# Kernel tuning notes

Measured on AMD Instinct MI355X. Metric: run time of the kernel, lower is better.

## Reference

```python
import jax, jax.numpy as jnp
import numpy as np

BS, S, DIM, H = 4, 2048, 768, 12
DH = DIM // H  # 64


def setup_inputs() -> dict:
    key = jax.random.key(0)
    ks = jax.random.split(key, 12)
    std = 0.02
    inp = {
        "query": jax.random.normal(ks[0], (BS, S, DIM), jnp.float32),
        "key_t": jax.random.normal(ks[1], (BS, S, DIM), jnp.float32),
        "value": jax.random.normal(ks[2], (BS, S, DIM), jnp.float32),
        "mask": jnp.ones((BS, S), jnp.int32),
        "q_w": jax.random.normal(ks[3], (DIM, DIM), jnp.float32) * std,
        "q_b": jnp.zeros((DIM,), jnp.float32),
        "k_w": jax.random.normal(ks[4], (DIM, DIM), jnp.float32) * std,
        "k_b": jnp.zeros((DIM,), jnp.float32),
        "v_w": jax.random.normal(ks[5], (DIM, DIM), jnp.float32) * std,
        "v_b": jnp.zeros((DIM,), jnp.float32),
        "o_w": jax.random.normal(ks[6], (DIM, DIM), jnp.float32) * std,
        "o_b": jnp.zeros((DIM,), jnp.float32),
    }
    return inp


def _shape(x, bs):
    # (bs, L, dim) -> (bs, H, L, DH)
    return x.reshape(bs, -1, H, DH).transpose(0, 2, 1, 3)


def reference(query, key_t, value, mask, q_w, q_b, k_w, k_b, v_w, v_b, o_w, o_b):
    bs, q_len, _ = query.shape
    k_len = key_t.shape[1]
    q = _shape(query @ q_w.T + q_b, bs)   # (bs,H,Sq,DH)
    k = _shape(key_t @ k_w.T + k_b, bs)   # (bs,H,Sk,DH)
    v = _shape(value @ v_w.T + v_b, bs)
    q = q * (1.0 / jnp.sqrt(jnp.asarray(DH, q.dtype)))
    scores = jnp.einsum("bhqd,bhkd->bhqk", q, k)  # (bs,H,Sq,Sk)
    pad = (mask == 0)[:, None, None, :]           # (bs,1,1,Sk)
    neg = jnp.finfo(scores.dtype).min
    scores = jnp.where(pad, neg, scores)
    weights = jax.nn.softmax(scores, axis=-1)
    context = jnp.einsum("bhqk,bhkd->bhqd", weights, v)
    context = context.transpose(0, 2, 1, 3).reshape(bs, q_len, H * DH)
    out = context @ o_w.T + o_b
    return out
```

## Files before the change

kernel.cpp:

```cpp
#include <hip/hip_runtime.h>


#define BSZ 4
#define SEQ 2048
#define DIMD 768
#define NHD 12
#define MTOT (BSZ*SEQ)
#define WELEM (DIMD*DIMD)

typedef __bf16 bf16;
typedef __attribute__((ext_vector_type(8))) __bf16 bf16x8;
typedef __attribute__((ext_vector_type(4))) __bf16 bf16x4;
typedef __attribute__((ext_vector_type(4))) float f32x4;

__device__ __forceinline__ f32x4 mfma_bf16(bf16x8 a, bf16x8 b, f32x4 c) {
    return __builtin_amdgcn_mfma_f32_16x16x32_bf16(a, b, c, 0, 0, 0);
}

__device__ __forceinline__ void async16(const bf16* g, bf16* l) {
    __builtin_amdgcn_global_load_lds(
        (const __attribute__((address_space(1))) unsigned int*)g,
        (__attribute__((address_space(3))) unsigned int*)l, 16, 0, 0);
}

__global__ __launch_bounds__(256) void convert_w_kernel(
    const float* __restrict__ w0, const float* __restrict__ w1,
    const float* __restrict__ w2, const float* __restrict__ w3,
    bf16* __restrict__ out) {
    const int z = blockIdx.y;
    const float* src = (z == 0) ? w0 : (z == 1) ? w1 : (z == 2) ? w2 : w3;
    const int i = (blockIdx.x * 256 + threadIdx.x) * 4;
    float4 v = *(const float4*)(src + i);
    bf16x4 o;
    o[0] = (bf16)v.x; o[1] = (bf16)v.y; o[2] = (bf16)v.z; o[3] = (bf16)v.w;
    *(bf16x4*)(out + (size_t)z * WELEM + i) = o;
}

__global__ __launch_bounds__(256) void convert_x_kernel(
    const float* __restrict__ src, bf16* __restrict__ dst) {
    const int i = (blockIdx.x * 256 + threadIdx.x) * 4;
    float4 v = *(const float4*)(src + i);
    bf16x4 o;
    o[0] = (bf16)v.x; o[1] = (bf16)v.y; o[2] = (bf16)v.z; o[3] = (bf16)v.w;
    *(bf16x4*)(dst + i) = o;
}

__device__ __forceinline__ void gemm_core_768(
    const bf16* __restrict__ Ag, const bf16* __restrict__ Bg,
    int m0, int n0, bf16* As, bf16* Bs, f32x4 (&acc)[4][4]) {
    const int tid = threadIdx.x;
    const int lane = tid & 63, wv = tid >> 6;
    const int quad = lane >> 4, l16 = lane & 15;
    const int wr = wv >> 1, wc = wv & 1;
    const int rr = lane >> 3, cbl = lane & 7;
    const int swz = l16 & 7;
    for (int kt = 0; kt < 12; ++kt) {
        if (kt) __syncthreads();
        for (int c = 0; c < 4; ++c) {
            const int row = c * 32 + wv * 8 + rr;
            const int cb = cbl ^ (row & 7);
            const size_t gcol = (size_t)kt * 64 + cb * 8;
            async16(Ag + (size_t)(m0 + row) * 768 + gcol, As + row * 64 + cbl * 8);
            async16(Bg + (size_t)(n0 + row) * 768 + gcol, Bs + row * 64 + cbl * 8);
        }
        __syncthreads();
        for (int ks = 0; ks < 2; ++ks) {
            bf16x8 af[4], bfr[4];
            for (int t = 0; t < 4; ++t)
                af[t] = *(const bf16x8*)(As + (wr * 64 + t * 16 + l16) * 64 +
                                         (((ks * 4 + quad) ^ swz) * 8));
            for (int t = 0; t < 4; ++t)
                bfr[t] = *(const bf16x8*)(Bs + (wc * 64 + t * 16 + l16) * 64 +
                                          (((ks * 4 + quad) ^ swz) * 8));
            for (int ti = 0; ti < 4; ++ti)
                for (int tj = 0; tj < 4; ++tj)
                    acc[ti][tj] = mfma_bf16(af[ti], bfr[tj], acc[ti][tj]);
        }
    }
}

__global__ __launch_bounds__(256, 3) void proj_kernel(
    const bf16* __restrict__ X, const bf16* __restrict__ W,
    const float* __restrict__ bias, bf16* __restrict__ Out, int z) {
    __shared__ __align__(16) bf16 smem[2 * 128 * 64];
    bf16* As = smem;
    bf16* Bs = smem + 128 * 64;
    const int tid = threadIdx.x;
    const int lane = tid & 63, wv = tid >> 6;
    const int quad = lane >> 4, l16 = lane & 15;
    const int wr = wv >> 1, wc = wv & 1;
    f32x4 acc[4][4] = {};
    int m0, n0;
    const bf16 *Ag, *Bg;
    if (z < 2) { m0 = blockIdx.y * 128; n0 = blockIdx.x * 128; Ag = W; Bg = X; }
    else       { m0 = blockIdx.x * 128; n0 = blockIdx.y * 128; Ag = X; Bg = W; }
    gemm_core_768(Ag, Bg, m0, n0, As, Bs, acc);
    __syncthreads();
    bf16* Ot = smem;
    if (z < 2) {
        const float scale = (z == 0) ? 0.125f : 1.0f;
        for (int ti = 0; ti < 4; ++ti) {
            const int featl = wr * 64 + ti * 16 + quad * 4;
            const float4 b4 = *(const float4*)(bias + m0 + featl);
            for (int tj = 0; tj < 4; ++tj) {
                const int sl = wc * 64 + tj * 16 + l16;
                bf16x4 pk;
                pk[0] = (bf16)((acc[ti][tj][0] + b4.x) * scale);
                pk[1] = (bf16)((acc[ti][tj][1] + b4.y) * scale);
                pk[2] = (bf16)((acc[ti][tj][2] + b4.z) * scale);
                pk[3] = (bf16)((acc[ti][tj][3] + b4.w) * scale);
                *(bf16x4*)&Ot[sl * 128 + featl] = pk;
            }
        }
        __syncthreads();
        for (int it = 0; it < 8; ++it) {
            const int unit = it * 256 + tid;
            const int s = unit >> 4, u = unit & 15;
            const int feat = m0 + u * 8;
            const int hh = feat >> 6, dh = feat & 63;
            const int srow = n0 + s;
            const int bb = srow >> 11, s2 = srow & 2047;
            *(bf16x8*)&Out[((size_t)(bb * NHD + hh) * SEQ + s2) * 64 + dh] =
                *(const bf16x8*)&Ot[s * 128 + u * 8];
        }
    } else {
        for (int ti = 0; ti < 4; ++ti) {
            const int sl = wr * 64 + ti * 16 + quad * 4;
            for (int tj = 0; tj < 4; ++tj) {
                const int featl = wc * 64 + tj * 16 + l16;
                const float bv = bias[n0 + featl];
                bf16x4 pk;
                pk[0] = (bf16)(acc[ti][tj][0] + bv);
                pk[1] = (bf16)(acc[ti][tj][1] + bv);
                pk[2] = (bf16)(acc[ti][tj][2] + bv);
                pk[3] = (bf16)(acc[ti][tj][3] + bv);
                *(bf16x4*)&Ot[featl * 128 + sl] = pk;
            }
        }
        __syncthreads();
        const int bb = m0 >> 11, sbase = m0 & 2047;
        for (int it = 0; it < 8; ++it) {
            const int unit = it * 256 + tid;
            const int fl = unit >> 4, u = unit & 15;
            const int feat = n0 + fl;
            const int hh = feat >> 6, dh = feat & 63;
            *(bf16x8*)&Out[((size_t)(bb * NHD + hh) * 64 + dh) * SEQ + sbase + u * 8] =
                *(const bf16x8*)&Ot[fl * 128 + u * 8];
        }
    }
}

__global__ __launch_bounds__(256, 3) void attn_kernel(
    const bf16* __restrict__ Qb, const bf16* __restrict__ Kb, const bf16* __restrict__ Vb,
    const int* __restrict__ mask, bf16* __restrict__ CTX) {
    __shared__ __align__(16) bf16 Ps[2][128][72];
    __shared__ float alphas[2][128];
    __shared__ float sadd[2048];
    __shared__ float invs[128];
    __shared__ int anyz_s;
    const int tid = threadIdx.x;
    const int lane = tid & 63, wv = tid >> 6, quad = lane >> 4, l16 = lane & 15;
    const int b = blockIdx.z, h = blockIdx.y, qt = blockIdx.x;
    const int bh = b * NHD + h;
    if (tid == 0) anyz_s = 0;
    __syncthreads();
    {
        int4 m0v = *(const int4*)(mask + b * SEQ + tid * 8);
        int4 m1v = *(const int4*)(mask + b * SEQ + tid * 8 + 4);
        float4 f0, f1;
        f0.x = m0v.x ? 0.f : -1e30f; f0.y = m0v.y ? 0.f : -1e30f;
        f0.z = m0v.z ? 0.f : -1e30f; f0.w = m0v.w ? 0.f : -1e30f;
        f1.x = m1v.x ? 0.f : -1e30f; f1.y = m1v.y ? 0.f : -1e30f;
        f1.z = m1v.z ? 0.f : -1e30f; f1.w = m1v.w ? 0.f : -1e30f;
        *(float4*)&sadd[tid * 8] = f0;
        *(float4*)&sadd[tid * 8 + 4] = f1;
        if (!(m0v.x && m0v.y && m0v.z && m0v.w && m1v.x && m1v.y && m1v.z && m1v.w))
            anyz_s = 1;
    }
    bf16x8 qf0[2], qf1[2];
    for (int st = 0; st < 2; ++st) {
        const bf16* qp = Qb + ((size_t)bh * SEQ + qt * 128 + wv * 32 + st * 16 + l16) * 64;
        qf0[st] = *(const bf16x8*)(qp + quad * 8);
        qf1[st] = *(const bf16x8*)(qp + 32 + quad * 8);
    }
    const bf16* Kp = Kb + (size_t)bh * SEQ * 64 + (size_t)l16 * 64 + quad * 8;
    const bf16* Vp = Vb + (size_t)bh * 64 * SEQ + (size_t)(wv * 16 + l16) * SEQ + quad * 8;
    f32x4 acc_o[8] = {};
    float rm[2] = {-1e30f, -1e30f}, rs[2] = {0.f, 0.f};
    __syncthreads();
    const int az = anyz_s;
    for (int kt = 0; kt < SEQ / 64; ++kt) {
        const int buf = kt & 1, k0 = kt * 64;
        bf16x8 kf0[4], kf1[4];
        for (int jj = 0; jj < 4; ++jj) {
            const bf16* kp = Kp + (size_t)(k0 + jj * 16) * 64;
            kf0[jj] = *(const bf16x8*)kp;
            kf1[jj] = *(const bf16x8*)(kp + 32);
        }
        f32x4 sc[2][4];
        for (int st = 0; st < 2; ++st)
            for (int jj = 0; jj < 4; ++jj) {
                f32x4 zf = {};
                zf = mfma_bf16(kf0[jj], qf0[st], zf);
                sc[st][jj] = mfma_bf16(kf1[jj], qf1[st], zf);
            }
        if (az)
            for (int jj = 0; jj < 4; ++jj) {
                const float4 sa = *(const float4*)&sadd[k0 + jj * 16 + quad * 4];
                for (int st = 0; st < 2; ++st) {
                    sc[st][jj][0] += sa.x; sc[st][jj][1] += sa.y;
                    sc[st][jj][2] += sa.z; sc[st][jj][3] += sa.w;
                }
            }
        for (int st = 0; st < 2; ++st) {
            float tmax = -1e30f;
            for (int jj = 0; jj < 4; ++jj)
                for (int r = 0; r < 4; ++r) tmax = fmaxf(tmax, sc[st][jj][r]);
            tmax = fmaxf(tmax, __shfl_xor(tmax, 16));
            tmax = fmaxf(tmax, __shfl_xor(tmax, 32));
            const float nmax = fmaxf(rm[st], tmax);
            const float alpha = __expf(rm[st] - nmax);
            rm[st] = nmax;
            float tsum = 0.f;
            for (int jj = 0; jj < 4; ++jj) {
                bf16x4 pk;
                for (int r = 0; r < 4; ++r) {
                    const float p = __expf(sc[st][jj][r] - nmax);
                    tsum += p;
                    pk[r] = (bf16)p;
                }
                *(bf16x4*)&Ps[buf][wv * 32 + st * 16 + l16][jj * 16 + quad * 4] = pk;
            }
            tsum += __shfl_xor(tsum, 16);
            tsum += __shfl_xor(tsum, 32);
            rs[st] = rs[st] * alpha + tsum;
            if (lane < 16) alphas[buf][wv * 32 + st * 16 + lane] = alpha;
        }
        bf16x8 vf0 = *(const bf16x8*)(Vp + k0);
        bf16x8 vf1 = *(const bf16x8*)(Vp + k0 + 32);
        __syncthreads();
        for (int qj = 0; qj < 8; ++qj) {
            const float al = alphas[buf][qj * 16 + l16];
            f32x4 c = acc_o[qj];
            c[0] *= al; c[1] *= al; c[2] *= al; c[3] *= al;
            bf16x8 pf0 = *(const bf16x8*)&Ps[buf][qj * 16 + l16][quad * 8];
            bf16x8 pf1 = *(const bf16x8*)&Ps[buf][qj * 16 + l16][32 + quad * 8];
            c = mfma_bf16(vf0, pf0, c);
            c = mfma_bf16(vf1, pf1, c);
            acc_o[qj] = c;
        }
    }
    if (lane < 16) {
        invs[wv * 32 + lane] = 1.0f / rs[0];
        invs[wv * 32 + 16 + lane] = 1.0f / rs[1];
    }
    __syncthreads();
    for (int qj = 0; qj < 8; ++qj) {
        const float inv = invs[qj * 16 + l16];
        bf16x4 pk;
        for (int r = 0; r < 4; ++r) pk[r] = (bf16)(acc_o[qj][r] * inv);
        const int s = qt * 128 + qj * 16 + l16;
        *(bf16x4*)&CTX[(size_t)(b * SEQ + s) * DIMD + h * 64 + wv * 16 + quad * 4] = pk;
    }
}

__global__ __launch_bounds__(256, 3) void oproj_kernel(
    const bf16* __restrict__ ctx, const bf16* __restrict__ wo,
    const float* __restrict__ bo, float* __restrict__ out) {
    __shared__ __align__(16) bf16 smem[2 * 128 * 64];
    const int tid = threadIdx.x;
    const int lane = tid & 63, wv = tid >> 6;
    const int quad = lane >> 4, l16 = lane & 15;
    const int wr = wv >> 1, wc = wv & 1;
    const int m0 = blockIdx.x * 128, n0 = blockIdx.y * 128;
    f32x4 acc[4][4] = {};
    gemm_core_768(ctx, wo, m0, n0, smem, smem + 128 * 64, acc);
    for (int ti = 0; ti < 4; ++ti) {
        const int rowb = m0 + wr * 64 + ti * 16 + quad * 4;
        for (int tj = 0; tj < 4; ++tj) {
            const int feat = n0 + wc * 64 + tj * 16 + l16;
            const float bv = bo[feat];
            for (int r = 0; r < 4; ++r)
                out[(size_t)(rowb + r) * DIMD + feat] = acc[ti][tj][r] + bv;
        }
    }
}

extern "C" void kernel_launch(void* const* d_in, const int* in_sizes, int n_in,
                              void* d_out, int out_size, void* d_ws, size_t ws_size,
                              hipStream_t stream) {
    const float* query = (const float*)d_in[0];
    const float* key_t = (const float*)d_in[1];
    const float* value = (const float*)d_in[2];
    const int*   mask  = (const int*)d_in[3];
    const float* q_w = (const float*)d_in[4];
    const float* q_b = (const float*)d_in[5];
    const float* k_w = (const float*)d_in[6];
    const float* k_b = (const float*)d_in[7];
    const float* v_w = (const float*)d_in[8];
    const float* v_b = (const float*)d_in[9];
    const float* o_w = (const float*)d_in[10];
    const float* o_b = (const float*)d_in[11];
    float* out = (float*)d_out;

    bf16* ws  = (bf16*)d_ws;
    bf16* W   = ws;
    bf16* XB  = ws + (size_t)4 * WELEM;
    bf16* Qb  = XB + (size_t)MTOT * DIMD;
    bf16* Kb  = Qb + (size_t)MTOT * DIMD;
    bf16* Vb  = Kb + (size_t)MTOT * DIMD;
    bf16* CTX = XB;

    convert_w_kernel<<<dim3(WELEM / 1024, 4), 256, 0, stream>>>(q_w, k_w, v_w, o_w, W);

    convert_x_kernel<<<MTOT * DIMD / 1024, 256, 0, stream>>>(query, XB);
    proj_kernel<<<dim3(64, 6), 256, 0, stream>>>(XB, W, q_b, Qb, 0);
    convert_x_kernel<<<MTOT * DIMD / 1024, 256, 0, stream>>>(key_t, XB);
    proj_kernel<<<dim3(64, 6), 256, 0, stream>>>(XB, W + (size_t)WELEM, k_b, Kb, 1);
    convert_x_kernel<<<MTOT * DIMD / 1024, 256, 0, stream>>>(value, XB);
    proj_kernel<<<dim3(64, 6), 256, 0, stream>>>(XB, W + (size_t)2 * WELEM, v_b, Vb, 2);

    attn_kernel<<<dim3(SEQ / 128, NHD, BSZ), 256, 0, stream>>>(Qb, Kb, Vb, mask, CTX);
    oproj_kernel<<<dim3(64, 6), 256, 0, stream>>>(CTX, W + (size_t)3 * WELEM, o_b, out);
}
```

Measured before the change: 333.1 us.

## Batch QKV projections, prefetch K/V in attention, swizzle GEMM block order

```diff
diff --git a/kernel.cpp b/kernel.cpp
--- a/kernel.cpp
+++ b/kernel.cpp
@@ -37,7 +37,12 @@
 }
 
 __global__ __launch_bounds__(256) void convert_x_kernel(
-    const float* __restrict__ src, bf16* __restrict__ dst) {
+    const float* __restrict__ x0, const float* __restrict__ x1,
+    const float* __restrict__ x2,
+    bf16* __restrict__ d0, bf16* __restrict__ d1, bf16* __restrict__ d2) {
+    const int z = blockIdx.y;
+    const float* src = (z == 0) ? x0 : (z == 1) ? x1 : x2;
+    bf16* dst = (z == 0) ? d0 : (z == 1) ? d1 : d2;
     const int i = (blockIdx.x * 256 + threadIdx.x) * 4;
     float4 v = *(const float4*)(src + i);
     bf16x4 o;
@@ -80,11 +85,24 @@
 }
 
 __global__ __launch_bounds__(256, 3) void proj_kernel(
-    const bf16* __restrict__ X, const bf16* __restrict__ W,
-    const float* __restrict__ bias, bf16* __restrict__ Out, int z) {
+    const bf16* __restrict__ Xq, const bf16* __restrict__ Xk, const bf16* __restrict__ Xv,
+    const bf16* __restrict__ W,
+    const float* __restrict__ bq, const float* __restrict__ bk, const float* __restrict__ bv,
+    bf16* __restrict__ Qo, bf16* __restrict__ Ko, bf16* __restrict__ Vo) {
     __shared__ __align__(16) bf16 smem[2 * 128 * 64];
     bf16* As = smem;
     bf16* Bs = smem + 128 * 64;
+    const int lin = blockIdx.x;
+    const int swzb = (lin & 7) * 144 + (lin >> 3);
+    const int z = swzb / 384;
+    const int rem = swzb - z * 384;
+    const int rt = rem / 6;
+    const int xt = rem - rt * 6;
+    const bf16* X = (z == 0) ? Xq : (z == 1) ? Xk : Xv;
+    const bf16* Wz = W + (size_t)z * WELEM;
+    const float* bias = (z == 0) ? bq : (z == 1) ? bk : bv;
+    bf16* Out = (z == 0) ? Qo : (z == 1) ? Ko : Vo;
+
     const int tid = threadIdx.x;
     const int lane = tid & 63, wv = tid >> 6;
     const int quad = lane >> 4, l16 = lane & 15;
@@ -92,8 +110,8 @@
     f32x4 acc[4][4] = {};
     int m0, n0;
     const bf16 *Ag, *Bg;
-    if (z < 2) { m0 = blockIdx.y * 128; n0 = blockIdx.x * 128; Ag = W; Bg = X; }
-    else       { m0 = blockIdx.x * 128; n0 = blockIdx.y * 128; Ag = X; Bg = W; }
+    if (z < 2) { m0 = xt * 128; n0 = rt * 128; Ag = Wz; Bg = X; }
+    else       { m0 = rt * 128; n0 = xt * 128; Ag = X;  Bg = Wz; }
     gemm_core_768(Ag, Bg, m0, n0, As, Bs, acc);
     __syncthreads();
     bf16* Ot = smem;
@@ -155,7 +173,6 @@
     const int* __restrict__ mask, bf16* __restrict__ CTX) {
     __shared__ __align__(16) bf16 Ps[2][128][72];
     __shared__ float alphas[2][128];
-    __shared__ float sadd[2048];
     __shared__ float invs[128];
     __shared__ int anyz_s;
     const int tid = threadIdx.x;
@@ -167,13 +184,6 @@
     {
         int4 m0v = *(const int4*)(mask + b * SEQ + tid * 8);
         int4 m1v = *(const int4*)(mask + b * SEQ + tid * 8 + 4);
-        float4 f0, f1;
-        f0.x = m0v.x ? 0.f : -1e30f; f0.y = m0v.y ? 0.f : -1e30f;
-        f0.z = m0v.z ? 0.f : -1e30f; f0.w = m0v.w ? 0.f : -1e30f;
-        f1.x = m1v.x ? 0.f : -1e30f; f1.y = m1v.y ? 0.f : -1e30f;
-        f1.z = m1v.z ? 0.f : -1e30f; f1.w = m1v.w ? 0.f : -1e30f;
-        *(float4*)&sadd[tid * 8] = f0;
-        *(float4*)&sadd[tid * 8 + 4] = f1;
         if (!(m0v.x && m0v.y && m0v.z && m0v.w && m1v.x && m1v.y && m1v.z && m1v.w))
             anyz_s = 1;
     }
@@ -185,71 +195,97 @@
     }
     const bf16* Kp = Kb + (size_t)bh * SEQ * 64 + (size_t)l16 * 64 + quad * 8;
     const bf16* Vp = Vb + (size_t)bh * 64 * SEQ + (size_t)(wv * 16 + l16) * SEQ + quad * 8;
+    const int* Mp = mask + b * SEQ;
     f32x4 acc_o[8] = {};
     float rm[2] = {-1e30f, -1e30f}, rs[2] = {0.f, 0.f};
     __syncthreads();
     const int az = anyz_s;
-    for (int kt = 0; kt < SEQ / 64; ++kt) {
-        const int buf = kt & 1, k0 = kt * 64;
-        bf16x8 kf0[4], kf1[4];
-        for (int jj = 0; jj < 4; ++jj) {
-            const bf16* kp = Kp + (size_t)(k0 + jj * 16) * 64;
-            kf0[jj] = *(const bf16x8*)kp;
-            kf1[jj] = *(const bf16x8*)(kp + 32);
-        }
-        f32x4 sc[2][4];
-        for (int st = 0; st < 2; ++st)
-            for (int jj = 0; jj < 4; ++jj) {
-                f32x4 zf = {};
-                zf = mfma_bf16(kf0[jj], qf0[st], zf);
-                sc[st][jj] = mfma_bf16(kf1[jj], qf1[st], zf);
-            }
-        if (az)
-            for (int jj = 0; jj < 4; ++jj) {
-                const float4 sa = *(const float4*)&sadd[k0 + jj * 16 + quad * 4];
-                for (int st = 0; st < 2; ++st) {
-                    sc[st][jj][0] += sa.x; sc[st][jj][1] += sa.y;
-                    sc[st][jj][2] += sa.z; sc[st][jj][3] += sa.w;
-                }
-            }
-        for (int st = 0; st < 2; ++st) {
-            float tmax = -1e30f;
-            for (int jj = 0; jj < 4; ++jj)
-                for (int r = 0; r < 4; ++r) tmax = fmaxf(tmax, sc[st][jj][r]);
-            tmax = fmaxf(tmax, __shfl_xor(tmax, 16));
-            tmax = fmaxf(tmax, __shfl_xor(tmax, 32));
-            const float nmax = fmaxf(rm[st], tmax);
-            const float alpha = __expf(rm[st] - nmax);
-            rm[st] = nmax;
-            float tsum = 0.f;
-            for (int jj = 0; jj < 4; ++jj) {
-                bf16x4 pk;
-                for (int r = 0; r < 4; ++r) {
-                    const float p = __expf(sc[st][jj][r] - nmax);
-                    tsum += p;
-                    pk[r] = (bf16)p;
-                }
-                *(bf16x4*)&Ps[buf][wv * 32 + st * 16 + l16][jj * 16 + quad * 4] = pk;
-            }
-            tsum += __shfl_xor(tsum, 16);
-            tsum += __shfl_xor(tsum, 32);
-            rs[st] = rs[st] * alpha + tsum;
-            if (lane < 16) alphas[buf][wv * 32 + st * 16 + lane] = alpha;
-        }
-        bf16x8 vf0 = *(const bf16x8*)(Vp + k0);
-        bf16x8 vf1 = *(const bf16x8*)(Vp + k0 + 32);
-        __syncthreads();
-        for (int qj = 0; qj < 8; ++qj) {
-            const float al = alphas[buf][qj * 16 + l16];
-            f32x4 c = acc_o[qj];
-            c[0] *= al; c[1] *= al; c[2] *= al; c[3] *= al;
-            bf16x8 pf0 = *(const bf16x8*)&Ps[buf][qj * 16 + l16][quad * 8];
-            bf16x8 pf1 = *(const bf16x8*)&Ps[buf][qj * 16 + l16][32 + quad * 8];
-            c = mfma_bf16(vf0, pf0, c);
-            c = mfma_bf16(vf1, pf1, c);
-            acc_o[qj] = c;
-        }
-    }
+
+    bf16x8 kfa0[4], kfa1[4], vfa0, vfa1;
+    bf16x8 kfb0[4], kfb1[4], vfb0, vfb1;
+    for (int jj = 0; jj < 4; ++jj) {
+        const bf16* kp = Kp + (size_t)(jj * 16) * 64;
+        kfa0[jj] = *(const bf16x8*)kp;
+        kfa1[jj] = *(const bf16x8*)(kp + 32);
+    }
+    vfa0 = *(const bf16x8*)Vp;
+    vfa1 = *(const bf16x8*)(Vp + 32);
+
+#define ATT_STEP(KT, KC0, KC1, VC0, VC1, KN0, KN1, VN0, VN1) do {                  \
+        const int kt_ = (KT);                                                      \
+        const int buf_ = kt_ & 1;                                                  \
+        const int k0_ = kt_ * 64;                                                  \
+        f32x4 sc[2][4];                                                            \
+        for (int st = 0; st < 2; ++st)                                             \
+            for (int jj = 0; jj < 4; ++jj) {                                       \
+                f32x4 zf = {};                                                     \
+                zf = mfma_bf16(KC0[jj], qf0[st], zf);                              \
+                sc[st][jj] = mfma_bf16(KC1[jj], qf1[st], zf);                      \
+            }                                                                      \
+        {     \
+            const int kn_ = (kt_ + 1 < SEQ / 64) ? (kt_ + 1) * 64 : kt_ * 64;      \
+            for (int jj = 0; jj < 4; ++jj) {                                       \
+                const bf16* kp_ = Kp + (size_t)(kn_ + jj * 16) * 64;               \
+                KN0[jj] = *(const bf16x8*)kp_;                                     \
+                KN1[jj] = *(const bf16x8*)(kp_ + 32);                              \
+            }                                                                      \
+            VN0 = *(const bf16x8*)(Vp + kn_);                                      \
+            VN1 = *(const bf16x8*)(Vp + kn_ + 32);                                 \
+        }                                                                          \
+        if (az)                                                                    \
+            for (int jj = 0; jj < 4; ++jj) {                                       \
+                const int4 mm = *(const int4*)(Mp + k0_ + jj * 16 + quad * 4);     \
+                float4 sa;                                                         \
+                sa.x = mm.x ? 0.f : -1e30f; sa.y = mm.y ? 0.f : -1e30f;            \
+                sa.z = mm.z ? 0.f : -1e30f; sa.w = mm.w ? 0.f : -1e30f;            \
+                for (int st = 0; st < 2; ++st) {                                   \
+                    sc[st][jj][0] += sa.x; sc[st][jj][1] += sa.y;                  \
+                    sc[st][jj][2] += sa.z; sc[st][jj][3] += sa.w;                  \
+                }                                                                  \
+            }                                                                      \
+        for (int st = 0; st < 2; ++st) {                                           \
+            float tmax = -1e30f;                                                   \
+            for (int jj = 0; jj < 4; ++jj)                                         \
+                for (int r = 0; r < 4; ++r) tmax = fmaxf(tmax, sc[st][jj][r]);     \
+            tmax = fmaxf(tmax, __shfl_xor(tmax, 16));                              \
+            tmax = fmaxf(tmax, __shfl_xor(tmax, 32));                              \
+            const float nmax = fmaxf(rm[st], tmax);                                \
+            const float alpha = __expf(rm[st] - nmax);                             \
+            rm[st] = nmax;                                                         \
+            float tsum = 0.f;                                                      \
+            for (int jj = 0; jj < 4; ++jj) {                                       \
+                bf16x4 pk;                                                         \
+                for (int r = 0; r < 4; ++r) {                                      \
+                    const float p = __expf(sc[st][jj][r] - nmax);                  \
+                    tsum += p;                                                     \
+                    pk[r] = (bf16)p;                                               \
+                }                                                                  \
+                *(bf16x4*)&Ps[buf_][wv * 32 + st * 16 + l16][jj * 16 + quad * 4] = pk; \
+            }                                                                      \
+            tsum += __shfl_xor(tsum, 16);                                          \
+            tsum += __shfl_xor(tsum, 32);                                          \
+            rs[st] = rs[st] * alpha + tsum;                                        \
+            if (lane < 16) alphas[buf_][wv * 32 + st * 16 + lane] = alpha;         \
+        }                                                                          \
+        __syncthreads();                              \
+        for (int qj = 0; qj < 8; ++qj) {                                           \
+            const float al = alphas[buf_][qj * 16 + l16];                          \
+            f32x4 c = acc_o[qj];                                                   \
+            c[0] *= al; c[1] *= al; c[2] *= al; c[3] *= al;                        \
+            bf16x8 pf0 = *(const bf16x8*)&Ps[buf_][qj * 16 + l16][quad * 8];       \
+            bf16x8 pf1 = *(const bf16x8*)&Ps[buf_][qj * 16 + l16][32 + quad * 8];  \
+            c = mfma_bf16(VC0, pf0, c);                                            \
+            c = mfma_bf16(VC1, pf1, c);                                            \
+            acc_o[qj] = c;                                                         \
+        }                                                                          \
+    } while (0)
+
+    for (int kt2 = 0; kt2 < SEQ / 128; ++kt2) {
+        ATT_STEP(kt2 * 2,     kfa0, kfa1, vfa0, vfa1, kfb0, kfb1, vfb0, vfb1);
+        ATT_STEP(kt2 * 2 + 1, kfb0, kfb1, vfb0, vfb1, kfa0, kfa1, vfa0, vfa1);
+    }
+#undef ATT_STEP
+
     if (lane < 16) {
         invs[wv * 32 + lane] = 1.0f / rs[0];
         invs[wv * 32 + 16 + lane] = 1.0f / rs[1];
@@ -268,11 +304,15 @@
     const bf16* __restrict__ ctx, const bf16* __restrict__ wo,
     const float* __restrict__ bo, float* __restrict__ out) {
     __shared__ __align__(16) bf16 smem[2 * 128 * 64];
+    const int lin = blockIdx.x;
+    const int swzb = (lin & 7) * 48 + (lin >> 3);
+    const int rt = swzb / 6;
+    const int xt = swzb - rt * 6;
     const int tid = threadIdx.x;
     const int lane = tid & 63, wv = tid >> 6;
     const int quad = lane >> 4, l16 = lane & 15;
     const int wr = wv >> 1, wc = wv & 1;
-    const int m0 = blockIdx.x * 128, n0 = blockIdx.y * 128;
+    const int m0 = rt * 128, n0 = xt * 128;
     f32x4 acc[4][4] = {};
     gemm_core_768(ctx, wo, m0, n0, smem, smem + 128 * 64, acc);
     for (int ti = 0; ti < 4; ++ti) {
@@ -305,21 +345,20 @@
 
     bf16* ws  = (bf16*)d_ws;
     bf16* W   = ws;
-    bf16* XB  = ws + (size_t)4 * WELEM;
-    bf16* Qb  = XB + (size_t)MTOT * DIMD;
+    bf16* XBq = ws + (size_t)4 * WELEM;
+    bf16* XBk = XBq + (size_t)MTOT * DIMD;
+    bf16* XBv = XBk + (size_t)MTOT * DIMD;
+    bf16* Qb  = XBv + (size_t)MTOT * DIMD;
     bf16* Kb  = Qb + (size_t)MTOT * DIMD;
     bf16* Vb  = Kb + (size_t)MTOT * DIMD;
-    bf16* CTX = XB;
+    bf16* CTX = XBq;
 
     convert_w_kernel<<<dim3(WELEM / 1024, 4), 256, 0, stream>>>(q_w, k_w, v_w, o_w, W);
-
-    convert_x_kernel<<<MTOT * DIMD / 1024, 256, 0, stream>>>(query, XB);
-    proj_kernel<<<dim3(64, 6), 256, 0, stream>>>(XB, W, q_b, Qb, 0);
-    convert_x_kernel<<<MTOT * DIMD / 1024, 256, 0, stream>>>(key_t, XB);
-    proj_kernel<<<dim3(64, 6), 256, 0, stream>>>(XB, W + (size_t)WELEM, k_b, Kb, 1);
-    convert_x_kernel<<<MTOT * DIMD / 1024, 256, 0, stream>>>(value, XB);
-    proj_kernel<<<dim3(64, 6), 256, 0, stream>>>(XB, W + (size_t)2 * WELEM, v_b, Vb, 2);
+    convert_x_kernel<<<dim3(MTOT * DIMD / 1024, 3), 256, 0, stream>>>(
+        query, key_t, value, XBq, XBk, XBv);
+
+    proj_kernel<<<1152, 256, 0, stream>>>(XBq, XBk, XBv, W, q_b, k_b, v_b, Qb, Kb, Vb);
 
     attn_kernel<<<dim3(SEQ / 128, NHD, BSZ), 256, 0, stream>>>(Qb, Kb, Vb, mask, CTX);
-    oproj_kernel<<<dim3(64, 6), 256, 0, stream>>>(CTX, W + (size_t)3 * WELEM, o_b, out);
-}
+    oproj_kernel<<<384, 256, 0, stream>>>(CTX, W + (size_t)3 * WELEM, o_b, out);
+}
```

Result: faster. 312.5 us (-6.2%).

## Batch QKV projections, XCD-swizzle block order, per-wave attention without block syncs

Applied to the files above, without the earlier changes.

```diff
diff --git a/kernel.cpp b/kernel.cpp
--- a/kernel.cpp
+++ b/kernel.cpp
@@ -37,7 +37,12 @@
 }
 
 __global__ __launch_bounds__(256) void convert_x_kernel(
-    const float* __restrict__ src, bf16* __restrict__ dst) {
+    const float* __restrict__ x0, const float* __restrict__ x1,
+    const float* __restrict__ x2,
+    bf16* __restrict__ d0, bf16* __restrict__ d1, bf16* __restrict__ d2) {
+    const int z = blockIdx.y;
+    const float* src = (z == 0) ? x0 : (z == 1) ? x1 : x2;
+    bf16* dst = (z == 0) ? d0 : (z == 1) ? d1 : d2;
     const int i = (blockIdx.x * 256 + threadIdx.x) * 4;
     float4 v = *(const float4*)(src + i);
     bf16x4 o;
@@ -80,11 +85,24 @@
 }
 
 __global__ __launch_bounds__(256, 3) void proj_kernel(
-    const bf16* __restrict__ X, const bf16* __restrict__ W,
-    const float* __restrict__ bias, bf16* __restrict__ Out, int z) {
+    const bf16* __restrict__ Xq, const bf16* __restrict__ Xk, const bf16* __restrict__ Xv,
+    const bf16* __restrict__ W,
+    const float* __restrict__ bq, const float* __restrict__ bk, const float* __restrict__ bv,
+    bf16* __restrict__ Qo, bf16* __restrict__ Ko, bf16* __restrict__ Vo) {
     __shared__ __align__(16) bf16 smem[2 * 128 * 64];
     bf16* As = smem;
     bf16* Bs = smem + 128 * 64;
+    const int lin = blockIdx.x;
+    const int swzb = (lin & 7) * 144 + (lin >> 3);
+    const int z = swzb / 384;
+    const int rem = swzb - z * 384;
+    const int rt = rem / 6;
+    const int xt = rem - rt * 6;
+    const bf16* X = (z == 0) ? Xq : (z == 1) ? Xk : Xv;
+    const bf16* Wz = W + (size_t)z * WELEM;
+    const float* bias = (z == 0) ? bq : (z == 1) ? bk : bv;
+    bf16* Out = (z == 0) ? Qo : (z == 1) ? Ko : Vo;
+
     const int tid = threadIdx.x;
     const int lane = tid & 63, wv = tid >> 6;
     const int quad = lane >> 4, l16 = lane & 15;
@@ -92,8 +110,8 @@
     f32x4 acc[4][4] = {};
     int m0, n0;
     const bf16 *Ag, *Bg;
-    if (z < 2) { m0 = blockIdx.y * 128; n0 = blockIdx.x * 128; Ag = W; Bg = X; }
-    else       { m0 = blockIdx.x * 128; n0 = blockIdx.y * 128; Ag = X; Bg = W; }
+    if (z < 2) { m0 = xt * 128; n0 = rt * 128; Ag = Wz; Bg = X; }
+    else       { m0 = rt * 128; n0 = xt * 128; Ag = X;  Bg = Wz; }
     gemm_core_768(Ag, Bg, m0, n0, As, Bs, acc);
     __syncthreads();
     bf16* Ot = smem;
@@ -153,27 +171,20 @@
 __global__ __launch_bounds__(256, 3) void attn_kernel(
     const bf16* __restrict__ Qb, const bf16* __restrict__ Kb, const bf16* __restrict__ Vb,
     const int* __restrict__ mask, bf16* __restrict__ CTX) {
-    __shared__ __align__(16) bf16 Ps[2][128][72];
-    __shared__ float alphas[2][128];
-    __shared__ float sadd[2048];
-    __shared__ float invs[128];
+    __shared__ __align__(16) bf16 Ps[4][32][72];
     __shared__ int anyz_s;
     const int tid = threadIdx.x;
     const int lane = tid & 63, wv = tid >> 6, quad = lane >> 4, l16 = lane & 15;
-    const int b = blockIdx.z, h = blockIdx.y, qt = blockIdx.x;
-    const int bh = b * NHD + h;
+    const int lin = blockIdx.x;
+    const int nb = (lin & 7) * 96 + (lin >> 3);
+    const int qt = nb & 15;
+    const int bh = nb >> 4;
+    const int b = bh / NHD, h = bh - b * NHD;
     if (tid == 0) anyz_s = 0;
     __syncthreads();
     {
         int4 m0v = *(const int4*)(mask + b * SEQ + tid * 8);
         int4 m1v = *(const int4*)(mask + b * SEQ + tid * 8 + 4);
-        float4 f0, f1;
-        f0.x = m0v.x ? 0.f : -1e30f; f0.y = m0v.y ? 0.f : -1e30f;
-        f0.z = m0v.z ? 0.f : -1e30f; f0.w = m0v.w ? 0.f : -1e30f;
-        f1.x = m1v.x ? 0.f : -1e30f; f1.y = m1v.y ? 0.f : -1e30f;
-        f1.z = m1v.z ? 0.f : -1e30f; f1.w = m1v.w ? 0.f : -1e30f;
-        *(float4*)&sadd[tid * 8] = f0;
-        *(float4*)&sadd[tid * 8 + 4] = f1;
         if (!(m0v.x && m0v.y && m0v.z && m0v.w && m1v.x && m1v.y && m1v.z && m1v.w))
             anyz_s = 1;
     }
@@ -184,83 +195,105 @@
         qf1[st] = *(const bf16x8*)(qp + 32 + quad * 8);
     }
     const bf16* Kp = Kb + (size_t)bh * SEQ * 64 + (size_t)l16 * 64 + quad * 8;
-    const bf16* Vp = Vb + (size_t)bh * 64 * SEQ + (size_t)(wv * 16 + l16) * SEQ + quad * 8;
-    f32x4 acc_o[8] = {};
+    const bf16* Vp = Vb + (size_t)bh * 64 * SEQ + (size_t)l16 * SEQ + quad * 8;
+    const int* Mp = mask + b * SEQ;
+    bf16* Pw = &Ps[wv][0][0];
+    f32x4 acc[2][4] = {};
     float rm[2] = {-1e30f, -1e30f}, rs[2] = {0.f, 0.f};
     __syncthreads();
     const int az = anyz_s;
+
     for (int kt = 0; kt < SEQ / 64; ++kt) {
-        const int buf = kt & 1, k0 = kt * 64;
+        const int k0 = kt * 64;
         bf16x8 kf0[4], kf1[4];
+        #pragma unroll
         for (int jj = 0; jj < 4; ++jj) {
             const bf16* kp = Kp + (size_t)(k0 + jj * 16) * 64;
             kf0[jj] = *(const bf16x8*)kp;
             kf1[jj] = *(const bf16x8*)(kp + 32);
         }
-        f32x4 sc[2][4];
-        for (int st = 0; st < 2; ++st)
+        bf16x8 vf[4][2];
+        #pragma unroll
+        for (int d = 0; d < 4; ++d)
+            #pragma unroll
+            for (int kb = 0; kb < 2; ++kb)
+                vf[d][kb] = *(const bf16x8*)(Vp + (size_t)d * 16 * SEQ + k0 + kb * 32);
+        #pragma unroll
+        for (int st = 0; st < 2; ++st) {
+            f32x4 sc[4];
+            #pragma unroll
             for (int jj = 0; jj < 4; ++jj) {
                 f32x4 zf = {};
                 zf = mfma_bf16(kf0[jj], qf0[st], zf);
-                sc[st][jj] = mfma_bf16(kf1[jj], qf1[st], zf);
-            }
-        if (az)
-            for (int jj = 0; jj < 4; ++jj) {
-                const float4 sa = *(const float4*)&sadd[k0 + jj * 16 + quad * 4];
-                for (int st = 0; st < 2; ++st) {
-                    sc[st][jj][0] += sa.x; sc[st][jj][1] += sa.y;
-                    sc[st][jj][2] += sa.z; sc[st][jj][3] += sa.w;
+                sc[jj] = mfma_bf16(kf1[jj], qf1[st], zf);
+            }
+            if (az) {
+                #pragma unroll
+                for (int jj = 0; jj < 4; ++jj) {
+                    const int4 mm = *(const int4*)(Mp + k0 + jj * 16 + quad * 4);
+                    sc[jj][0] += mm.x ? 0.f : -1e30f;
+                    sc[jj][1] += mm.y ? 0.f : -1e30f;
+                    sc[jj][2] += mm.z ? 0.f : -1e30f;
+                    sc[jj][3] += mm.w ? 0.f : -1e30f;
                 }
             }
-        for (int st = 0; st < 2; ++st) {
             float tmax = -1e30f;
+            #pragma unroll
             for (int jj = 0; jj < 4; ++jj)
-                for (int r = 0; r < 4; ++r) tmax = fmaxf(tmax, sc[st][jj][r]);
+                #pragma unroll
+                for (int r = 0; r < 4; ++r) tmax = fmaxf(tmax, sc[jj][r]);
             tmax = fmaxf(tmax, __shfl_xor(tmax, 16));
             tmax = fmaxf(tmax, __shfl_xor(tmax, 32));
             const float nmax = fmaxf(rm[st], tmax);
             const float alpha = __expf(rm[st] - nmax);
             rm[st] = nmax;
             float tsum = 0.f;
+            #pragma unroll
             for (int jj = 0; jj < 4; ++jj) {
                 bf16x4 pk;
+                #pragma unroll
                 for (int r = 0; r < 4; ++r) {
-                    const float p = __expf(sc[st][jj][r] - nmax);
+                    const float p = __expf(sc[jj][r] - nmax);
                     tsum += p;
                     pk[r] = (bf16)p;
                 }
-                *(bf16x4*)&Ps[buf][wv * 32 + st * 16 + l16][jj * 16 + quad * 4] = pk;
+                *(bf16x4*)&Pw[(st * 16 + l16) * 72 + jj * 16 + quad * 4] = pk;
             }
             tsum += __shfl_xor(tsum, 16);
             tsum += __shfl_xor(tsum, 32);
             rs[st] = rs[st] * alpha + tsum;
-            if (lane < 16) alphas[buf][wv * 32 + st * 16 + lane] = alpha;
-        }
-        bf16x8 vf0 = *(const bf16x8*)(Vp + k0);
-        bf16x8 vf1 = *(const bf16x8*)(Vp + k0 + 32);
-        __syncthreads();
-        for (int qj = 0; qj < 8; ++qj) {
-            const float al = alphas[buf][qj * 16 + l16];
-            f32x4 c = acc_o[qj];
-            c[0] *= al; c[1] *= al; c[2] *= al; c[3] *= al;
-            bf16x8 pf0 = *(const bf16x8*)&Ps[buf][qj * 16 + l16][quad * 8];
-            bf16x8 pf1 = *(const bf16x8*)&Ps[buf][qj * 16 + l16][32 + quad * 8];
-            c = mfma_bf16(vf0, pf0, c);
-            c = mfma_bf16(vf1, pf1, c);
-            acc_o[qj] = c;
-        }
-    }
-    if (lane < 16) {
-        invs[wv * 32 + lane] = 1.0f / rs[0];
-        invs[wv * 32 + 16 + lane] = 1.0f / rs[1];
-    }
-    __syncthreads();
-    for (int qj = 0; qj < 8; ++qj) {
-        const float inv = invs[qj * 16 + l16];
-        bf16x4 pk;
-        for (int r = 0; r < 4; ++r) pk[r] = (bf16)(acc_o[qj][r] * inv);
-        const int s = qt * 128 + qj * 16 + l16;
-        *(bf16x4*)&CTX[(size_t)(b * SEQ + s) * DIMD + h * 64 + wv * 16 + quad * 4] = pk;
+            #pragma unroll
+            for (int d = 0; d < 4; ++d) {
+                acc[st][d][0] *= alpha; acc[st][d][1] *= alpha;
+                acc[st][d][2] *= alpha; acc[st][d][3] *= alpha;
+            }
+        }
+        bf16x8 pf[2][2];
+        #pragma unroll
+        for (int st = 0; st < 2; ++st)
+            #pragma unroll
+            for (int kb = 0; kb < 2; ++kb)
+                pf[st][kb] = *(const bf16x8*)&Pw[(st * 16 + l16) * 72 + kb * 32 + quad * 8];
+        #pragma unroll
+        for (int st = 0; st < 2; ++st)
+            #pragma unroll
+            for (int kb = 0; kb < 2; ++kb)
+                #pragma unroll
+                for (int d = 0; d < 4; ++d)
+                    acc[st][d] = mfma_bf16(vf[d][kb], pf[st][kb], acc[st][d]);
+    }
+
+    #pragma unroll
+    for (int st = 0; st < 2; ++st) {
+        const float inv = 1.0f / rs[st];
+        const int s = qt * 128 + wv * 32 + st * 16 + l16;
+        #pragma unroll
+        for (int d = 0; d < 4; ++d) {
+            bf16x4 pk;
+            #pragma unroll
+            for (int r = 0; r < 4; ++r) pk[r] = (bf16)(acc[st][d][r] * inv);
+            *(bf16x4*)&CTX[(size_t)(b * SEQ + s) * DIMD + h * 64 + d * 16 + quad * 4] = pk;
+        }
     }
 }
 
@@ -268,11 +301,15 @@
     const bf16* __restrict__ ctx, const bf16* __restrict__ wo,
     const float* __restrict__ bo, float* __restrict__ out) {
     __shared__ __align__(16) bf16 smem[2 * 128 * 64];
+    const int lin = blockIdx.x;
+    const int swzb = (lin & 7) * 48 + (lin >> 3);
+    const int rt = swzb / 6;
+    const int xt = swzb - rt * 6;
     const int tid = threadIdx.x;
     const int lane = tid & 63, wv = tid >> 6;
     const int quad = lane >> 4, l16 = lane & 15;
     const int wr = wv >> 1, wc = wv & 1;
-    const int m0 = blockIdx.x * 128, n0 = blockIdx.y * 128;
+    const int m0 = rt * 128, n0 = xt * 128;
     f32x4 acc[4][4] = {};
     gemm_core_768(ctx, wo, m0, n0, smem, smem + 128 * 64, acc);
     for (int ti = 0; ti < 4; ++ti) {
@@ -305,21 +342,20 @@
 
     bf16* ws  = (bf16*)d_ws;
     bf16* W   = ws;
-    bf16* XB  = ws + (size_t)4 * WELEM;
-    bf16* Qb  = XB + (size_t)MTOT * DIMD;
+    bf16* XBq = ws + (size_t)4 * WELEM;
+    bf16* XBk = XBq + (size_t)MTOT * DIMD;
+    bf16* XBv = XBk + (size_t)MTOT * DIMD;
+    bf16* Qb  = XBv + (size_t)MTOT * DIMD;
     bf16* Kb  = Qb + (size_t)MTOT * DIMD;
     bf16* Vb  = Kb + (size_t)MTOT * DIMD;
-    bf16* CTX = XB;
+    bf16* CTX = XBq;
 
     convert_w_kernel<<<dim3(WELEM / 1024, 4), 256, 0, stream>>>(q_w, k_w, v_w, o_w, W);
-
-    convert_x_kernel<<<MTOT * DIMD / 1024, 256, 0, stream>>>(query, XB);
-    proj_kernel<<<dim3(64, 6), 256, 0, stream>>>(XB, W, q_b, Qb, 0);
-    convert_x_kernel<<<MTOT * DIMD / 1024, 256, 0, stream>>>(key_t, XB);
-    proj_kernel<<<dim3(64, 6), 256, 0, stream>>>(XB, W + (size_t)WELEM, k_b, Kb, 1);
-    convert_x_kernel<<<MTOT * DIMD / 1024, 256, 0, stream>>>(value, XB);
-    proj_kernel<<<dim3(64, 6), 256, 0, stream>>>(XB, W + (size_t)2 * WELEM, v_b, Vb, 2);
-
-    attn_kernel<<<dim3(SEQ / 128, NHD, BSZ), 256, 0, stream>>>(Qb, Kb, Vb, mask, CTX);
-    oproj_kernel<<<dim3(64, 6), 256, 0, stream>>>(CTX, W + (size_t)3 * WELEM, o_b, out);
-}
+    convert_x_kernel<<<dim3(MTOT * DIMD / 1024, 3), 256, 0, stream>>>(
+        query, key_t, value, XBq, XBk, XBv);
+
+    proj_kernel<<<1152, 256, 0, stream>>>(XBq, XBk, XBv, W, q_b, k_b, v_b, Qb, Kb, Vb);
+
+    attn_kernel<<<768, 256, 0, stream>>>(Qb, Kb, Vb, mask, CTX);
+    oproj_kernel<<<384, 256, 0, stream>>>(CTX, W + (size_t)3 * WELEM, o_b, out);
+}
```

New measurement: 368.0 us. 10.5% more time.
